# Performance work log

Measured on AMD Instinct MI355X. Metric: run time of the kernel, lower is better.

Reference implementation:

```python
import jax, jax.numpy as jnp
import numpy as np

B, T, D, H, L, O = 256, 512, 64, 256, 2, 4


def _lstm_layer(x_tbd, W_ih, W_hh, b_ih, b_hh):
    """x_tbd: (T, B, D_in) -> hidden sequence (T, B, H). PyTorch gate order i,f,g,o."""
    Bb = x_tbd.shape[1]
    Hh = W_hh.shape[1]
    b = b_ih + b_hh
    # precompute input projections for all timesteps in one GEMM
    xW = jnp.einsum('tbd,gd->tbg', x_tbd, W_ih) + b  # (T, B, 4H)

    def step(carry, xw_t):
        h, c = carry
        gates = xw_t + h @ W_hh.T
        i, f, g, o = jnp.split(gates, 4, axis=-1)
        i = jax.nn.sigmoid(i)
        f = jax.nn.sigmoid(f)
        g = jnp.tanh(g)
        o = jax.nn.sigmoid(o)
        c = f * c + i * g
        h = o * jnp.tanh(c)
        return (h, c), h

    init = (jnp.zeros((Bb, Hh), x_tbd.dtype), jnp.zeros((Bb, Hh), x_tbd.dtype))
    _, hs = jax.lax.scan(step, init, xW)
    return hs


def setup_inputs() -> dict:
    key = jax.random.key(0)
    ks = jax.random.split(key, 11)
    s = 1.0 / np.sqrt(H)  # PyTorch LSTM init scale
    inp = {
        'x': jax.random.normal(ks[0], (B, T, D), dtype=jnp.float32),
        'W_ih0': jax.random.uniform(ks[1], (4 * H, D), minval=-s, maxval=s, dtype=jnp.float32),
        'W_hh0': jax.random.uniform(ks[2], (4 * H, H), minval=-s, maxval=s, dtype=jnp.float32),
        'b_ih0': jax.random.uniform(ks[3], (4 * H,), minval=-s, maxval=s, dtype=jnp.float32),
        'b_hh0': jax.random.uniform(ks[4], (4 * H,), minval=-s, maxval=s, dtype=jnp.float32),
        'W_ih1': jax.random.uniform(ks[5], (4 * H, H), minval=-s, maxval=s, dtype=jnp.float32),
        'W_hh1': jax.random.uniform(ks[6], (4 * H, H), minval=-s, maxval=s, dtype=jnp.float32),
        'b_ih1': jax.random.uniform(ks[7], (4 * H,), minval=-s, maxval=s, dtype=jnp.float32),
        'b_hh1': jax.random.uniform(ks[8], (4 * H,), minval=-s, maxval=s, dtype=jnp.float32),
        'fc_W': jax.random.uniform(ks[9], (O, H), minval=-s, maxval=s, dtype=jnp.float32),
        'fc_b': jax.random.uniform(ks[10], (O,), minval=-s, maxval=s, dtype=jnp.float32),
    }
    return inp


def reference(x, W_ih0, W_hh0, b_ih0, b_hh0, W_ih1, W_hh1, b_ih1, b_hh1, fc_W, fc_b):
    xt = jnp.transpose(x, (1, 0, 2))            # (T, B, D), batch_first -> time-major
    h1 = _lstm_layer(xt, W_ih0, W_hh0, b_ih0, b_hh0)   # (T, B, H)
    h2 = _lstm_layer(h1, W_ih1, W_hh1, b_ih1, b_hh1)   # (T, B, H)
    last = h2[-1]                                # out[:, -1, :] in batch_first layout
    return last @ fc_W.T + fc_b                  # (B, O)
```

## Files before the change

### kernel.cpp

```cpp
#include <hip/hip_runtime.h>


#define TT 512
#define HH 256
#define DD 64

typedef __attribute__((ext_vector_type(2))) _Float16 h2t;
typedef __attribute__((ext_vector_type(8))) _Float16 f16x8;
typedef __attribute__((ext_vector_type(4))) float f32x4;
typedef unsigned long long u64;

__device__ __forceinline__ unsigned pkh(float x, float y) {
    h2t h; h.x = (_Float16)x; h.y = (_Float16)y;
    return __builtin_bit_cast(unsigned, h);
}
__device__ __forceinline__ float sigf(float x) { return 1.f / (1.f + __expf(-x)); }
__device__ __forceinline__ float tanhf_(float x) {
    float e = __expf(2.f * x);
    return 1.f - 2.f / (e + 1.f);
}
__device__ __forceinline__ f16x8 ld8(const float* p) {
    float4 u = ((const float4*)p)[0];
    float4 v = ((const float4*)p)[1];
    f16x8 r = {(_Float16)u.x, (_Float16)u.y, (_Float16)u.z, (_Float16)u.w,
               (_Float16)v.x, (_Float16)v.y, (_Float16)v.z, (_Float16)v.w};
    return r;
}
__device__ __forceinline__ unsigned ldflag(const unsigned* p) {
    return __hip_atomic_load(p, __ATOMIC_RELAXED, __HIP_MEMORY_SCOPE_AGENT);
}
__device__ __forceinline__ u64 ld64(const u64* p) {
    return __hip_atomic_load(p, __ATOMIC_RELAXED, __HIP_MEMORY_SCOPE_AGENT);
}

__device__ __forceinline__ int phalf(int chunk, int row) {
    return (chunk * 16 + (row ^ (chunk & 7))) * 8;
}

#define DECLA(kt) f16x8 AK##kt##_0 = {}, AK##kt##_1 = {};

__global__ __launch_bounds__(512, 2) void lstm_persist(
    const float* __restrict__ x,
    const float* __restrict__ Wih0, const float* __restrict__ Whh0,
    const float* __restrict__ bih0, const float* __restrict__ bhh0,
    const float* __restrict__ Wih1, const float* __restrict__ Whh1,
    const float* __restrict__ bih1, const float* __restrict__ bhh1,
    const float* __restrict__ fcW, const float* __restrict__ fcb,
    float* __restrict__ out,
    unsigned short* h0buf, unsigned short* h1buf, unsigned* counters)
{
    __shared__ __align__(16) _Float16 sB[8192];
    __shared__ __align__(16) float part[8][272];

    const int tid   = threadIdx.x;
    const int g     = blockIdx.x & 31;
    const int role  = blockIdx.x >> 5;
    const bool isL1 = role >= 4;
    const int q     = role & 3;
    const int batch0 = g * 8;
    unsigned* flags = counters + (size_t)g * 16;

    const int lane = tid & 63;
    const int w    = tid >> 6;
    const int bcol = lane & 15;
    const int kc   = lane >> 4;
    const int koff = kc * 8;

    const int lr0 = w * 32 + (lane & 15);
    const int lr1 = lr0 + 16;
    const int R0  = 256 * (lr0 >> 6) + 64 * q + (lr0 & 63);
    const int R1  = 256 * (lr1 >> 6) + 64 * q + (lr1 & 63);

    DECLA(0) DECLA(1) DECLA(2) DECLA(3) DECLA(4) DECLA(5) DECLA(6) DECLA(7)
    DECLA(8) DECLA(9) DECLA(10) DECLA(11) DECLA(12) DECLA(13) DECLA(14) DECLA(15)

    if (isL1) {
#define LA1(kt) { const int k_ = (kt) * 32 + koff;                                   \
        AK##kt##_0 = ld8(((k_ < 256) ? Wih1 + (size_t)R0 * 256 + k_                  \
                                     : Whh1 + (size_t)R0 * 256 + (k_ - 256)));       \
        AK##kt##_1 = ld8(((k_ < 256) ? Wih1 + (size_t)R1 * 256 + k_                  \
                                     : Whh1 + (size_t)R1 * 256 + (k_ - 256))); }
        LA1(0) LA1(1) LA1(2) LA1(3) LA1(4) LA1(5) LA1(6) LA1(7)
        LA1(8) LA1(9) LA1(10) LA1(11) LA1(12) LA1(13) LA1(14) LA1(15)
#undef LA1
    } else {
#define LA0(kt) { const int k_ = (kt) * 32 + koff;                                   \
        AK##kt##_0 = ld8(((k_ < 64) ? Wih0 + (size_t)R0 * 64 + k_                    \
                                    : Whh0 + (size_t)R0 * 256 + (k_ - 64)));         \
        AK##kt##_1 = ld8(((k_ < 64) ? Wih0 + (size_t)R1 * 64 + k_                    \
                                    : Whh0 + (size_t)R1 * 256 + (k_ - 64))); }
        LA0(0) LA0(1) LA0(2) LA0(3) LA0(4) LA0(5) LA0(6) LA0(7) LA0(8) LA0(9)
#undef LA0
    }

    const float* bA = isL1 ? bih1 : bih0;
    const float* bB = isL1 ? bhh1 : bhh0;
    const float bz0 = bA[0 * 256 + 64 * q + lane] + bB[0 * 256 + 64 * q + lane];
    const float bz1 = bA[1 * 256 + 64 * q + lane] + bB[1 * 256 + 64 * q + lane];
    const float bz2 = bA[2 * 256 + 64 * q + lane] + bB[2 * 256 + 64 * q + lane];
    const float bz3 = bA[3 * 256 + 64 * q + lane] + bB[3 * 256 + 64 * q + lane];
    float cst = 0.f;

    {
        u64* z = (u64*)sB;
#pragma unroll
        for (int p = 0; p < 2; ++p) {
            int n = tid + p * 512;
            int c = n >> 4, rem = n & 15;
            z[(c * 16 + 8 + (rem >> 1)) * 2 + (rem & 1)] = 0;
        }
    }

    const u64* h0u = reinterpret_cast<const u64*>(h0buf);
    const u64* h1u = reinterpret_cast<const u64*>(h1buf);

    for (int s = 0; s <= TT; ++s) {
        const bool active = isL1 ? (s >= 1) : (s < TT);

        float4 xp;
        const bool doX = (!isL1) && (s < TT) && (tid >= 256) && (tid < 384);
        if (doX) {
            int t2 = tid - 256, j = t2 >> 4, c = t2 & 15;
            xp = reinterpret_cast<const float4*>(
                     x + ((size_t)(batch0 + j) * TT + s) * DD)[c];
        }

        if (s > 0 && tid < 8) {
            while (ldflag(&flags[tid]) < (unsigned)s) __builtin_amdgcn_s_sleep(1);
        }
        __syncthreads();

        if (active) {
            u64* z = (u64*)sB;
            const int b = tid >> 6, t = tid & 63;
            u64 hv = ld64(h0u + (size_t)((s + 1) & 1) * 16384 + batch0 * 64 + tid);
            z[phalf((isL1 ? 0 : 8) + (t >> 1), b) / 4 + (t & 1)] = hv;
            if (isL1) {
                u64 hv1 = ld64(h1u + (size_t)(s & 1) * 16384 + batch0 * 64 + tid);
                z[phalf(32 + (t >> 1), b) / 4 + (t & 1)] = hv1;
            } else if (doX) {
                int t2 = tid - 256, j = t2 >> 4, c = t2 & 15;
                u64 v = (u64)pkh(xp.x, xp.y) | ((u64)pkh(xp.z, xp.w) << 32);
                z[phalf(c >> 1, j) / 4 + (c & 1)] = v;
            }
        }
        __syncthreads();

        if (active) {
            f32x4 Ca = {0.f, 0.f, 0.f, 0.f}, Cb = {0.f, 0.f, 0.f, 0.f};
#define MK(kt) { const int ch_ = (kt) * 4 + kc;                                       \
        const f16x8 Bf = *(const f16x8*)(sB + phalf(ch_, bcol));                      \
        Ca = __builtin_amdgcn_mfma_f32_16x16x32_f16(AK##kt##_0, Bf, Ca, 0, 0, 0);     \
        Cb = __builtin_amdgcn_mfma_f32_16x16x32_f16(AK##kt##_1, Bf, Cb, 0, 0, 0); }
            if (isL1) {
                MK(0) MK(1) MK(2) MK(3) MK(4) MK(5) MK(6) MK(7)
                MK(8) MK(9) MK(10) MK(11) MK(12) MK(13) MK(14) MK(15)
            } else {
                MK(0) MK(1) MK(2) MK(3) MK(4) MK(5) MK(6) MK(7) MK(8) MK(9)
            }
#undef MK
            if (bcol < 8) {
                *(f32x4*)&part[bcol][w * 32 + kc * 4]      = Ca;
                *(f32x4*)&part[bcol][w * 32 + 16 + kc * 4] = Cb;
            }
        }
        __syncthreads();

        if (active) {
            float s0 = part[w][(0 << 6) | lane] + bz0;
            float s1 = part[w][(1 << 6) | lane] + bz1;
            float s2 = part[w][(2 << 6) | lane] + bz2;
            float s3 = part[w][(3 << 6) | lane] + bz3;
            float fi = sigf(s0), ff = sigf(s1), fg = tanhf_(s2), fo = sigf(s3);
            cst = ff * cst + fi * fg;
            float h = fo * tanhf_(cst);

            float hn = __shfl_down(h, 1);
            unsigned lo = pkh(h, hn);
            unsigned hi = __shfl_down(lo, 2);
            if ((lane & 3) == 0) {
                u64 v = (u64)lo | ((u64)hi << 32);
                unsigned short* base = isL1
                    ? h1buf + (size_t)((s - 1) & 1) * 65536
                    : h0buf + (size_t)(s & 1) * 65536;
                u64* dst = reinterpret_cast<u64*>(base + (size_t)(batch0 + w) * HH + 64 * q + lane);
                __hip_atomic_store(dst, v, __ATOMIC_RELAXED, __HIP_MEMORY_SCOPE_AGENT);
            }
        }
        asm volatile("s_waitcnt vmcnt(0)" ::: "memory");
        __syncthreads();

        if (tid == 0)
            __hip_atomic_store(&flags[role], (unsigned)(s + 1),
                               __ATOMIC_RELAXED, __HIP_MEMORY_SCOPE_AGENT);
    }

    if (isL1 && q == 0) {
        if (tid < 4) {
            while (ldflag(&flags[4 + tid]) < (unsigned)(TT + 1)) __builtin_amdgcn_s_sleep(1);
        }
        __syncthreads();
        ((u64*)sB)[tid] = ld64(h1u + 16384 + batch0 * 64 + tid);
        __syncthreads();

        const int j = tid >> 6, l2 = tid & 63;
        const int o = l2 >> 4, kk = l2 & 15;
        float ssum = 0.f;
#pragma unroll
        for (int m = 0; m < 16; ++m) {
            int k = kk * 16 + m;
            ssum += (float)sB[j * 256 + k] * fcW[o * HH + k];
        }
#pragma unroll
        for (int off = 8; off; off >>= 1) ssum += __shfl_down(ssum, off);
        if (kk == 0) out[(batch0 + j) * 4 + o] = ssum + fcb[o];
    }
}

extern "C" void kernel_launch(void* const* d_in, const int* in_sizes, int n_in,
                              void* d_out, int out_size, void* d_ws, size_t ws_size,
                              hipStream_t stream)
{
    (void)in_sizes; (void)n_in; (void)out_size; (void)ws_size;
    const float* x    = (const float*)d_in[0];
    const float* Wih0 = (const float*)d_in[1];
    const float* Whh0 = (const float*)d_in[2];
    const float* bih0 = (const float*)d_in[3];
    const float* bhh0 = (const float*)d_in[4];
    const float* Wih1 = (const float*)d_in[5];
    const float* Whh1 = (const float*)d_in[6];
    const float* bih1 = (const float*)d_in[7];
    const float* bhh1 = (const float*)d_in[8];
    const float* fcW  = (const float*)d_in[9];
    const float* fcb  = (const float*)d_in[10];
    float* out = (float*)d_out;

    unsigned short* h0buf = (unsigned short*)d_ws;
    unsigned short* h1buf = (unsigned short*)((char*)d_ws + 262144);
    unsigned*       cnts  = (unsigned*)((char*)d_ws + 524288);

    hipMemsetAsync(d_ws, 0, 524288 + 2048, stream);

    lstm_persist<<<dim3(256), dim3(512), 0, stream>>>(
        x, Wih0, Whh0, bih0, bhh0, Wih1, Whh1, bih1, bhh1, fcW, fcb, out,
        h0buf, h1buf, cnts);
}
```

Before: 1.391 ms.

## Replace per-step flag barriers with epoch-tagged ring buffers and K-split waves

Hidden-state exchange between blocks now goes through a 4-slot ring in which each 64-bit word carries an epoch tag next to the packed fp16 pair. Consumers spin on the tag itself instead of waiting on a per-block flag and then loading, and the staging for the next step is overlapped with the end of the current step. Flags are kept only as coarse back-pressure so producers do not overwrite ring slots that are still being read. The MFMA work is also re-split so each wave covers four M tiles over half of K, with partial sums reduced through LDS. This removes one barrier per step at the cost of more spinning global loads and a larger workspace.

```diff
diff --git a/kernel.cpp b/kernel.cpp
--- a/kernel.cpp
+++ b/kernel.cpp
@@ -9,10 +9,11 @@
 typedef __attribute__((ext_vector_type(8))) _Float16 f16x8;
 typedef __attribute__((ext_vector_type(4))) float f32x4;
 typedef unsigned long long u64;
-
-__device__ __forceinline__ unsigned pkh(float x, float y) {
+typedef unsigned u32;
+
+__device__ __forceinline__ u32 pkh(float x, float y) {
     h2t h; h.x = (_Float16)x; h.y = (_Float16)y;
-    return __builtin_bit_cast(unsigned, h);
+    return __builtin_bit_cast(u32, h);
 }
 __device__ __forceinline__ float sigf(float x) { return 1.f / (1.f + __expf(-x)); }
 __device__ __forceinline__ float tanhf_(float x) {
@@ -26,18 +27,18 @@
                (_Float16)v.x, (_Float16)v.y, (_Float16)v.z, (_Float16)v.w};
     return r;
 }
-__device__ __forceinline__ unsigned ldflag(const unsigned* p) {
+__device__ __forceinline__ u32 ld32(const u32* p) {
     return __hip_atomic_load(p, __ATOMIC_RELAXED, __HIP_MEMORY_SCOPE_AGENT);
+}
+__device__ __forceinline__ void st32(u32* p, u32 v) {
+    __hip_atomic_store(p, v, __ATOMIC_RELAXED, __HIP_MEMORY_SCOPE_AGENT);
 }
 __device__ __forceinline__ u64 ld64(const u64* p) {
     return __hip_atomic_load(p, __ATOMIC_RELAXED, __HIP_MEMORY_SCOPE_AGENT);
 }
-
-__device__ __forceinline__ int phalf(int chunk, int row) {
-    return (chunk * 16 + (row ^ (chunk & 7))) * 8;
-}
-
-#define DECLA(kt) f16x8 AK##kt##_0 = {}, AK##kt##_1 = {};
+__device__ __forceinline__ void st64(u64* p, u64 v) {
+    __hip_atomic_store(p, v, __ATOMIC_RELAXED, __HIP_MEMORY_SCOPE_AGENT);
+}
 
 __global__ __launch_bounds__(512, 2) void lstm_persist(
     const float* __restrict__ x,
@@ -47,162 +48,176 @@
     const float* __restrict__ bih1, const float* __restrict__ bhh1,
     const float* __restrict__ fcW, const float* __restrict__ fcb,
     float* __restrict__ out,
-    unsigned short* h0buf, unsigned short* h1buf, unsigned* counters)
+    u64* h0ring, u64* h1ring, u32* cflagsA)
 {
-    __shared__ __align__(16) _Float16 sB[8192];
-    __shared__ __align__(16) float part[8][272];
-
-    const int tid   = threadIdx.x;
-    const int g     = blockIdx.x & 31;
-    const int role  = blockIdx.x >> 5;
+    __shared__ __align__(16) _Float16 sB[9216];
+    __shared__ __align__(16) float part2[2][8][276];
+
+    const int tid  = threadIdx.x;
+    const int g    = blockIdx.x & 31;
+    const int role = blockIdx.x >> 5;
     const bool isL1 = role >= 4;
-    const int q     = role & 3;
+    const int q = role & 3;
     const int batch0 = g * 8;
-    unsigned* flags = counters + (size_t)g * 16;
-
-    const int lane = tid & 63;
-    const int w    = tid >> 6;
-    const int bcol = lane & 15;
-    const int kc   = lane >> 4;
-    const int koff = kc * 8;
-
-    const int lr0 = w * 32 + (lane & 15);
-    const int lr1 = lr0 + 16;
-    const int R0  = 256 * (lr0 >> 6) + 64 * q + (lr0 & 63);
-    const int R1  = 256 * (lr1 >> 6) + 64 * q + (lr1 & 63);
-
-    DECLA(0) DECLA(1) DECLA(2) DECLA(3) DECLA(4) DECLA(5) DECLA(6) DECLA(7)
-    DECLA(8) DECLA(9) DECLA(10) DECLA(11) DECLA(12) DECLA(13) DECLA(14) DECLA(15)
+    u64* ring0 = h0ring + (size_t)g * 4096;
+    u64* ring1 = h1ring + (size_t)g * 4096;
+    u32* cflag = cflagsA + (size_t)g * 16;
+
+    const int lane = tid & 63, w = tid >> 6;
+    const int mw = w & 3, kh = w >> 2;
+    const int bcol = lane & 15, kc = lane >> 4;
+
+    const int R0 = mw * 256 + 64 * q + (lane & 15);
+    const int R1 = R0 + 16, R2 = R0 + 32, R3 = R0 + 48;
+
+#define DECL_TI(ti) f16x8 A##ti##_0={},A##ti##_1={},A##ti##_2={},A##ti##_3={}, \
+                          A##ti##_4={},A##ti##_5={},A##ti##_6={},A##ti##_7={};
+    DECL_TI(0) DECL_TI(1) DECL_TI(2) DECL_TI(3)
+#undef DECL_TI
 
     if (isL1) {
-#define LA1(kt) { const int k_ = (kt) * 32 + koff;                                   \
-        AK##kt##_0 = ld8(((k_ < 256) ? Wih1 + (size_t)R0 * 256 + k_                  \
-                                     : Whh1 + (size_t)R0 * 256 + (k_ - 256)));       \
-        AK##kt##_1 = ld8(((k_ < 256) ? Wih1 + (size_t)R1 * 256 + k_                  \
-                                     : Whh1 + (size_t)R1 * 256 + (k_ - 256))); }
-        LA1(0) LA1(1) LA1(2) LA1(3) LA1(4) LA1(5) LA1(6) LA1(7)
-        LA1(8) LA1(9) LA1(10) LA1(11) LA1(12) LA1(13) LA1(14) LA1(15)
-#undef LA1
+#define LDA1(ti,j) { int k_ = (kh*8+(j))*32 + kc*8;                          \
+        A##ti##_##j = ld8(k_ < 256 ? Wih1 + (size_t)R##ti*256 + k_           \
+                                   : Whh1 + (size_t)R##ti*256 + (k_-256)); }
+#define LDA1T(ti) LDA1(ti,0) LDA1(ti,1) LDA1(ti,2) LDA1(ti,3) \
+                  LDA1(ti,4) LDA1(ti,5) LDA1(ti,6) LDA1(ti,7)
+        LDA1T(0) LDA1T(1) LDA1T(2) LDA1T(3)
+#undef LDA1T
+#undef LDA1
     } else {
-#define LA0(kt) { const int k_ = (kt) * 32 + koff;                                   \
-        AK##kt##_0 = ld8(((k_ < 64) ? Wih0 + (size_t)R0 * 64 + k_                    \
-                                    : Whh0 + (size_t)R0 * 256 + (k_ - 64)));         \
-        AK##kt##_1 = ld8(((k_ < 64) ? Wih0 + (size_t)R1 * 64 + k_                    \
-                                    : Whh0 + (size_t)R1 * 256 + (k_ - 64))); }
-        LA0(0) LA0(1) LA0(2) LA0(3) LA0(4) LA0(5) LA0(6) LA0(7) LA0(8) LA0(9)
-#undef LA0
+#define LDA0(ti,j) { int k_ = (kh*5+(j))*32 + kc*8;                          \
+        A##ti##_##j = ld8(k_ < 64 ? Wih0 + (size_t)R##ti*64 + k_             \
+                                  : Whh0 + (size_t)R##ti*256 + (k_-64)); }
+#define LDA0T(ti) LDA0(ti,0) LDA0(ti,1) LDA0(ti,2) LDA0(ti,3) LDA0(ti,4)
+        LDA0T(0) LDA0T(1) LDA0T(2) LDA0T(3)
+#undef LDA0T
+#undef LDA0
     }
 
     const float* bA = isL1 ? bih1 : bih0;
     const float* bB = isL1 ? bhh1 : bhh0;
-    const float bz0 = bA[0 * 256 + 64 * q + lane] + bB[0 * 256 + 64 * q + lane];
-    const float bz1 = bA[1 * 256 + 64 * q + lane] + bB[1 * 256 + 64 * q + lane];
-    const float bz2 = bA[2 * 256 + 64 * q + lane] + bB[2 * 256 + 64 * q + lane];
-    const float bz3 = bA[3 * 256 + 64 * q + lane] + bB[3 * 256 + 64 * q + lane];
+    const float bz0 = bA[      64*q + lane] + bB[      64*q + lane];
+    const float bz1 = bA[256 + 64*q + lane] + bB[256 + 64*q + lane];
+    const float bz2 = bA[512 + 64*q + lane] + bB[512 + 64*q + lane];
+    const float bz3 = bA[768 + 64*q + lane] + bB[768 + 64*q + lane];
     float cst = 0.f;
 
-    {
-        u64* z = (u64*)sB;
-#pragma unroll
-        for (int p = 0; p < 2; ++p) {
-            int n = tid + p * 512;
-            int c = n >> 4, rem = n & 15;
-            z[(c * 16 + 8 + (rem >> 1)) * 2 + (rem & 1)] = 0;
-        }
-    }
-
-    const u64* h0u = reinterpret_cast<const u64*>(h0buf);
-    const u64* h1u = reinterpret_cast<const u64*>(h1buf);
+    u32* const sBu = (u32*)sB;
+    for (int i = tid; i < 4608; i += 512) sBu[i] = 0;
+
+    auto stage_next = [&](int snext) {
+        const bool st0 = (!isL1) && (snext < TT);
+        const bool st1 = isL1 && (snext >= 1) && (snext <= TT);
+        if (!(st0 || st1)) return;
+        {
+            const int slot = (snext - 1) & 3;
+            const u32 e0 = (u32)snext;
+            const int base = isL1 ? 0 : 8;
+#pragma unroll
+            for (int pp = 0; pp < 2; ++pp) {
+                int p = tid + pp * 512;
+                int j = p >> 7, n = p & 127;
+                const u64* a = ring0 + slot * 1024 + (n >> 5) * 256 + j * 32 + (n & 31);
+                u64 v;
+                do { v = ld64(a); } while ((u32)(v >> 32) != e0);
+                sBu[(base + (n >> 2)) * 72 + j * 4 + (n & 3)] = (u32)v;
+            }
+        }
+        if (isL1) {
+            const int slot = (snext + 2) & 3;
+            const u32 e1 = (snext >= 2) ? (u32)snext : 0u;
+#pragma unroll
+            for (int pp = 0; pp < 2; ++pp) {
+                int p = tid + pp * 512;
+                int j = p >> 7, n = p & 127;
+                const u64* a = ring1 + slot * 1024 + (n >> 5) * 256 + j * 32 + (n & 31);
+                u64 v;
+                do { v = ld64(a); } while ((u32)(v >> 32) != e1);
+                sBu[(32 + (n >> 2)) * 72 + j * 4 + (n & 3)] = (u32)v;
+            }
+        } else if (tid >= 256 && tid < 384) {
+            int t2 = tid - 256, j = t2 >> 4, c = t2 & 15;
+            float4 v = ((const float4*)(x + ((size_t)(batch0 + j) * TT + snext) * DD))[c];
+            int bidx = (c >> 1) * 72 + j * 4 + (c & 1) * 2;
+            sBu[bidx]     = pkh(v.x, v.y);
+            sBu[bidx + 1] = pkh(v.z, v.w);
+        }
+    };
+    stage_next(0);
 
     for (int s = 0; s <= TT; ++s) {
-        const bool active = isL1 ? (s >= 1) : (s < TT);
-
-        float4 xp;
-        const bool doX = (!isL1) && (s < TT) && (tid >= 256) && (tid < 384);
-        if (doX) {
-            int t2 = tid - 256, j = t2 >> 4, c = t2 & 15;
-            xp = reinterpret_cast<const float4*>(
-                     x + ((size_t)(batch0 + j) * TT + s) * DD)[c];
-        }
-
-        if (s > 0 && tid < 8) {
-            while (ldflag(&flags[tid]) < (unsigned)s) __builtin_amdgcn_s_sleep(1);
-        }
         __syncthreads();
-
-        if (active) {
-            u64* z = (u64*)sB;
-            const int b = tid >> 6, t = tid & 63;
-            u64 hv = ld64(h0u + (size_t)((s + 1) & 1) * 16384 + batch0 * 64 + tid);
-            z[phalf((isL1 ? 0 : 8) + (t >> 1), b) / 4 + (t & 1)] = hv;
+        if (tid == 0) st32(&cflag[role], (u32)(s + 1));
+
+        const bool act_ = isL1 ? (s >= 1) : (s < TT);
+
+        u32 cpre = 0xFFFFFFFFu;
+        if (act_ && lane < 8) cpre = ld32(&cflag[lane]);
+
+        if (act_) {
+            f32x4 C0 = {0,0,0,0}, C1 = {0,0,0,0}, C2 = {0,0,0,0}, C3 = {0,0,0,0};
+#define MST(j, ktb) { const f16x8 Bf = *(const f16x8*)(sB + (((ktb)+(j))*4 + kc)*144 + bcol*8); \
+            C0 = __builtin_amdgcn_mfma_f32_16x16x32_f16(A0_##j, Bf, C0, 0,0,0); \
+            C1 = __builtin_amdgcn_mfma_f32_16x16x32_f16(A1_##j, Bf, C1, 0,0,0); \
+            C2 = __builtin_amdgcn_mfma_f32_16x16x32_f16(A2_##j, Bf, C2, 0,0,0); \
+            C3 = __builtin_amdgcn_mfma_f32_16x16x32_f16(A3_##j, Bf, C3, 0,0,0); }
             if (isL1) {
-                u64 hv1 = ld64(h1u + (size_t)(s & 1) * 16384 + batch0 * 64 + tid);
-                z[phalf(32 + (t >> 1), b) / 4 + (t & 1)] = hv1;
-            } else if (doX) {
-                int t2 = tid - 256, j = t2 >> 4, c = t2 & 15;
-                u64 v = (u64)pkh(xp.x, xp.y) | ((u64)pkh(xp.z, xp.w) << 32);
-                z[phalf(c >> 1, j) / 4 + (c & 1)] = v;
+                const int ktb = kh * 8;
+                MST(0,ktb) MST(1,ktb) MST(2,ktb) MST(3,ktb)
+                MST(4,ktb) MST(5,ktb) MST(6,ktb) MST(7,ktb)
+            } else {
+                const int ktb = kh * 5;
+                MST(0,ktb) MST(1,ktb) MST(2,ktb) MST(3,ktb) MST(4,ktb)
+            }
+#undef MST
+            if (bcol < 8) {
+                *(f32x4*)&part2[kh][bcol][mw*64 +  0 + kc*4] = C0;
+                *(f32x4*)&part2[kh][bcol][mw*64 + 16 + kc*4] = C1;
+                *(f32x4*)&part2[kh][bcol][mw*64 + 32 + kc*4] = C2;
+                *(f32x4*)&part2[kh][bcol][mw*64 + 48 + kc*4] = C3;
             }
         }
         __syncthreads();
 
-        if (active) {
-            f32x4 Ca = {0.f, 0.f, 0.f, 0.f}, Cb = {0.f, 0.f, 0.f, 0.f};
-#define MK(kt) { const int ch_ = (kt) * 4 + kc;                                       \
-        const f16x8 Bf = *(const f16x8*)(sB + phalf(ch_, bcol));                      \
-        Ca = __builtin_amdgcn_mfma_f32_16x16x32_f16(AK##kt##_0, Bf, Ca, 0, 0, 0);     \
-        Cb = __builtin_amdgcn_mfma_f32_16x16x32_f16(AK##kt##_1, Bf, Cb, 0, 0, 0); }
-            if (isL1) {
-                MK(0) MK(1) MK(2) MK(3) MK(4) MK(5) MK(6) MK(7)
-                MK(8) MK(9) MK(10) MK(11) MK(12) MK(13) MK(14) MK(15)
-            } else {
-                MK(0) MK(1) MK(2) MK(3) MK(4) MK(5) MK(6) MK(7) MK(8) MK(9)
-            }
-#undef MK
-            if (bcol < 8) {
-                *(f32x4*)&part[bcol][w * 32 + kc * 4]      = Ca;
-                *(f32x4*)&part[bcol][w * 32 + 16 + kc * 4] = Cb;
-            }
-        }
-        __syncthreads();
-
-        if (active) {
-            float s0 = part[w][(0 << 6) | lane] + bz0;
-            float s1 = part[w][(1 << 6) | lane] + bz1;
-            float s2 = part[w][(2 << 6) | lane] + bz2;
-            float s3 = part[w][(3 << 6) | lane] + bz3;
+        if (act_) {
+            float s0 = part2[0][w][      lane] + part2[1][w][      lane] + bz0;
+            float s1 = part2[0][w][ 64 + lane] + part2[1][w][ 64 + lane] + bz1;
+            float s2 = part2[0][w][128 + lane] + part2[1][w][128 + lane] + bz2;
+            float s3 = part2[0][w][192 + lane] + part2[1][w][192 + lane] + bz3;
             float fi = sigf(s0), ff = sigf(s1), fg = tanhf_(s2), fo = sigf(s3);
             cst = ff * cst + fi * fg;
             float h = fo * tanhf_(cst);
-
             float hn = __shfl_down(h, 1);
-            unsigned lo = pkh(h, hn);
-            unsigned hi = __shfl_down(lo, 2);
-            if ((lane & 3) == 0) {
-                u64 v = (u64)lo | ((u64)hi << 32);
-                unsigned short* base = isL1
-                    ? h1buf + (size_t)((s - 1) & 1) * 65536
-                    : h0buf + (size_t)(s & 1) * 65536;
-                u64* dst = reinterpret_cast<u64*>(base + (size_t)(batch0 + w) * HH + 64 * q + lane);
-                __hip_atomic_store(dst, v, __ATOMIC_RELAXED, __HIP_MEMORY_SCOPE_AGENT);
-            }
-        }
-        asm volatile("s_waitcnt vmcnt(0)" ::: "memory");
+
+            const int tgt = s - 2;
+            while (!__all(lane >= 8 || (int)cpre >= tgt)) {
+                __builtin_amdgcn_s_sleep(1);
+                if (lane < 8) cpre = ld32(&cflag[lane]);
+            }
+            if (!(lane & 1)) {
+                u64 v = ((u64)(u32)(s + 1) << 32) | (u64)pkh(h, hn);
+                u64* dst = (isL1 ? ring1 + (size_t)((s - 1) & 3) * 1024
+                                 : ring0 + (size_t)(s & 3) * 1024)
+                           + q * 256 + w * 32 + (lane >> 1);
+                st64(dst, v);
+            }
+        }
+
+        stage_next(s + 1);
+    }
+
+    if (isL1 && q == 0) {
+        const u32 ef = (u32)(TT + 1);
+#pragma unroll
+        for (int pp = 0; pp < 2; ++pp) {
+            int p = tid + pp * 512;
+            int j = p >> 7, n = p & 127;
+            const u64* a = ring1 + 3 * 1024 + (n >> 5) * 256 + j * 32 + (n & 31);
+            u64 v;
+            do { v = ld64(a); } while ((u32)(v >> 32) != ef);
+            sBu[j * 128 + n] = (u32)v;
+        }
         __syncthreads();
-
-        if (tid == 0)
-            __hip_atomic_store(&flags[role], (unsigned)(s + 1),
-                               __ATOMIC_RELAXED, __HIP_MEMORY_SCOPE_AGENT);
-    }
-
-    if (isL1 && q == 0) {
-        if (tid < 4) {
-            while (ldflag(&flags[4 + tid]) < (unsigned)(TT + 1)) __builtin_amdgcn_s_sleep(1);
-        }
-        __syncthreads();
-        ((u64*)sB)[tid] = ld64(h1u + 16384 + batch0 * 64 + tid);
-        __syncthreads();
-
         const int j = tid >> 6, l2 = tid & 63;
         const int o = l2 >> 4, kk = l2 & 15;
         float ssum = 0.f;
@@ -235,13 +250,13 @@
     const float* fcb  = (const float*)d_in[10];
     float* out = (float*)d_out;
 
-    unsigned short* h0buf = (unsigned short*)d_ws;
-    unsigned short* h1buf = (unsigned short*)((char*)d_ws + 262144);
-    unsigned*       cnts  = (unsigned*)((char*)d_ws + 524288);
-
-    hipMemsetAsync(d_ws, 0, 524288 + 2048, stream);
+    u64* h0ring = (u64*)d_ws;
+    u64* h1ring = (u64*)((char*)d_ws + 1048576);
+    u32* cflags = (u32*)((char*)d_ws + 2097152);
+
+    hipMemsetAsync(d_ws, 0, 2097152 + 2048, stream);
 
     lstm_persist<<<dim3(256), dim3(512), 0, stream>>>(
         x, Wih0, Whh0, bih0, bhh0, Wih1, Whh1, bih1, bhh1, fcW, fcb, out,
-        h0buf, h1buf, cnts);
-}
+        h0ring, h1ring, cflags);
+}
```

Result: faster. 1.278 ms (-8.1%).
